# Kernel tuning notes

Hardware: AMD Instinct MI355X
Metric: run time of the kernel (lower is better)

The kernel has to match this reference:

```python
import jax, jax.numpy as jnp
import numpy as np
import math

B, N, DIM, H, D, M = 2, 2048, 512, 8, 64, 128  # batch, seq, model dim, heads, head_dim, num_features


def _sample_orf(head_dim, num_features, seed=0):
    """Orthogonal random features with chi(d) norm scaling (FAVOR+), numpy host-side."""
    rng = np.random.default_rng(seed)
    blocks = []
    while len(blocks) * head_dim < num_features:
        G = rng.standard_normal((head_dim, head_dim)).astype(np.float32)
        Q, _ = np.linalg.qr(G)
        norms = np.linalg.norm(rng.standard_normal((head_dim, head_dim)).astype(np.float32), axis=1)
        blocks.append(np.diag(norms) @ Q.T)
    return np.concatenate(blocks, axis=0)[:num_features]


def setup_inputs() -> dict:
    key = jax.random.key(0)
    ks = jax.random.split(key, 6)
    inner = H * D
    x = jax.random.normal(ks[0], (B, N, DIM), dtype=jnp.float32)
    s = DIM ** -0.5
    Wq = jax.random.normal(ks[1], (inner, DIM), dtype=jnp.float32) * s
    Wk = jax.random.normal(ks[2], (inner, DIM), dtype=jnp.float32) * s
    Wv = jax.random.normal(ks[3], (inner, DIM), dtype=jnp.float32) * s
    Wo = jax.random.normal(ks[4], (DIM, inner), dtype=jnp.float32) * (inner ** -0.5)
    bo = jax.random.normal(ks[5], (DIM,), dtype=jnp.float32) * 0.01
    omega = jnp.asarray(_sample_orf(D, M), dtype=jnp.float32)  # [M, D]
    return {"x": x, "omega": omega, "Wq": Wq, "Wk": Wk, "Wv": Wv, "Wo": Wo, "bo": bo}


def _phi(x, omega, is_query):
    # x: [B,H,N,D], omega: [M,D] -> [B,H,N,M]
    proj = jnp.einsum('bhnd,md->bhnm', x, omega)
    log_phi = proj - 0.5 * jnp.sum(x * x, axis=-1, keepdims=True)
    if is_query:
        log_phi = log_phi - jnp.max(log_phi, axis=-1, keepdims=True)
    else:
        log_phi = log_phi - jnp.max(log_phi)
    return jnp.exp(log_phi) / math.sqrt(M) + 1e-4


def reference(x, omega, Wq, Wk, Wv, Wo, bo):
    # projections: torch Linear is y = x @ W.T
    q = (x @ Wq.T).reshape(B, N, H, D).transpose(0, 2, 1, 3)  # [B,H,N,D]
    k = (x @ Wk.T).reshape(B, N, H, D).transpose(0, 2, 1, 3)
    v = (x @ Wv.T).reshape(B, N, H, D).transpose(0, 2, 1, 3)
    scale = D ** -0.25
    phi_q = _phi(q * scale, omega, True)   # [B,H,N,M]
    phi_k = _phi(k * scale, omega, False)  # [B,H,N,M]

    # Causal linear attention as a recurrent scan over the sequence; math equals
    # cumsum of einsum('bhnm,bhnd->bhnmd') without the O(N*M*D) intermediate.
    def step(carry, inp):
        kv, ksum = carry                      # [B,H,M,D], [B,H,M]
        pqn, pkn, vn = inp                    # [B,H,M], [B,H,M], [B,H,D]
        kv = kv + pkn[..., None] * vn[:, :, None, :]
        ksum = ksum + pkn
        o = jnp.einsum('bhm,bhmd->bhd', pqn, kv)
        z = 1.0 / (jnp.einsum('bhm,bhm->bh', pqn, ksum) + 1e-6)
        return (kv, ksum), o * z[..., None]

    init = (jnp.zeros((B, H, M, D), x.dtype), jnp.zeros((B, H, M), x.dtype))
    xs = (phi_q.transpose(2, 0, 1, 3), phi_k.transpose(2, 0, 1, 3), v.transpose(2, 0, 1, 3))
    _, outs = jax.lax.scan(step, init, xs)    # outs: [N,B,H,D]
    out = outs.transpose(1, 0, 2, 3).reshape(B, N, H * D)
    return out @ Wo.T + bo
```

## Files before the change

kernel.cpp:

```cpp
#include <hip/hip_runtime.h>
#include <math.h>

#define B_ 2
#define N_ 2048
#define DIM_ 512
#define H_ 8
#define D_ 64
#define M_ 128
#define NC_ 32
#define C_ 64

#define INV_SQRT_M 0.08838834764831845f
#define QK_SCALE 0.35355339059327373f

typedef __attribute__((ext_vector_type(8))) short bf16x8;
typedef __attribute__((ext_vector_type(4))) short bf16x4;
typedef __attribute__((ext_vector_type(4))) float f32x4;

#define MFMA16(a, b, c) __builtin_amdgcn_mfma_f32_16x16x32_bf16((a), (b), (c), 0, 0, 0)

__device__ __forceinline__ short f2bf(float f) {
    union { float f; unsigned u; } x; x.f = f;
    unsigned r = (x.u + 0x7FFFu + ((x.u >> 16) & 1u)) >> 16;
    return (short)r;
}
__device__ __forceinline__ float bf2f(short s) {
    union { unsigned u; float f; } x; x.u = ((unsigned)(unsigned short)s) << 16;
    return x.f;
}
__device__ __forceinline__ unsigned encf(float f) {
    unsigned u = __float_as_uint(f);
    return (u & 0x80000000u) ? ~u : (u | 0x80000000u);
}
__device__ __forceinline__ float decf(unsigned e) {
    unsigned u = (e & 0x80000000u) ? (e & 0x7FFFFFFFu) : ~e;
    return __uint_as_float(u);
}

__device__ __forceinline__ void gl16(void* lds, const void* g) {
    __builtin_amdgcn_global_load_lds(
        (const __attribute__((address_space(1))) unsigned int*)g,
        (__attribute__((address_space(3))) unsigned int*)lds,
        16, 0, 0);
}

__device__ __forceinline__ bf16x8 ld_frag(const short* base, int row0, int k0, int ldk) {
    const int lane = threadIdx.x & 63;
    return *(const bf16x8*)(base + (row0 + (lane & 15)) * ldk + k0 + ((lane >> 4) << 3));
}
__device__ __forceinline__ bf16x8 ld_fragT(const short* base, int col0, int k0, int ldk) {
    const int lane = threadIdx.x & 63;
    const short* p = base + (k0 + ((lane >> 4) << 3)) * ldk + col0 + (lane & 15);
    bf16x8 r;
    #pragma unroll
    for (int i = 0; i < 8; ++i) r[i] = p[i * ldk];
    return r;
}

__global__ __launch_bounds__(256) void prep(
    const float* __restrict__ x, const float* __restrict__ Wk, const float* __restrict__ Wv,
    const float* __restrict__ Wo,
    short* __restrict__ xh, short* __restrict__ xl,
    short* __restrict__ Wch, short* __restrict__ Woh, unsigned* __restrict__ gmaxu)
{
    int i4 = blockIdx.x * 256 + threadIdx.x;
    if (i4 == 0) gmaxu[0] = 0u;
    if (i4 < 524288) {
        float4 v = *(const float4*)(x + (size_t)i4 * 4);
        float a[4] = {v.x, v.y, v.z, v.w};
        bf16x4 hi, lo;
        #pragma unroll
        for (int u = 0; u < 4; ++u) {
            short h = f2bf(a[u]); hi[u] = h; lo[u] = f2bf(a[u] - bf2f(h));
        }
        *(bf16x4*)(xh + (size_t)i4 * 4) = hi;
        *(bf16x4*)(xl + (size_t)i4 * 4) = lo;
    } else if (i4 < 720896) {
        int r = i4 - 524288;
        int widx = r >> 16, off4 = r & 65535;
        const float* src; short* dst; float sc;
        if (widx == 0)      { src = Wk; dst = Wch;          sc = QK_SCALE; }
        else if (widx == 1) { src = Wv; dst = Wch + 262144; sc = 1.f; }
        else                { src = Wo; dst = Woh;          sc = 1.f; }
        float4 v = *(const float4*)(src + (size_t)off4 * 4);
        bf16x4 hi;
        hi[0] = f2bf(v.x * sc); hi[1] = f2bf(v.y * sc);
        hi[2] = f2bf(v.z * sc); hi[3] = f2bf(v.w * sc);
        *(bf16x4*)(dst + (size_t)off4 * 4) = hi;
    }
}

__global__ __launch_bounds__(256) void prep_omw(const float* __restrict__ omega,
    const float* __restrict__ Wq, const float* __restrict__ Wk,
    short* __restrict__ Wch, short* __restrict__ Wcl)
{
    __shared__ float Ws[64][65];
    __shared__ float om[128][64];
    const int t = threadIdx.x;
    const int qk = blockIdx.x >> 6, h = (blockIdx.x >> 3) & 7, cb = blockIdx.x & 7;
    const int col0 = cb * 64;
    const float* W = qk ? Wk : Wq;
    for (int i = t; i < 64 * 64; i += 256) {
        int d = i >> 6, c = i & 63;
        Ws[d][c] = W[(size_t)(h * 64 + d) * 512 + col0 + c] * QK_SCALE;
    }
    for (int i = t; i < 128 * 64; i += 256) om[i >> 6][i & 63] = omega[i];
    __syncthreads();
    const int lane = t & 63, w = t >> 6;
    const int c = col0 + lane;
    float Wcol[64];
    #pragma unroll
    for (int d = 0; d < 64; ++d) Wcol[d] = Ws[d][lane];
    for (int mi = 0; mi < 32; ++mi) {
        int m = w * 32 + mi;
        float acc = 0.f;
        #pragma unroll
        for (int d = 0; d < 64; d += 4) {
            float4 o4 = *(const float4*)&om[m][d];
            acc += o4.x * Wcol[d] + o4.y * Wcol[d+1] + o4.z * Wcol[d+2] + o4.w * Wcol[d+3];
        }
        int row = 1024 + qk * 1024 + h * 128 + m;
        short hi = f2bf(acc);
        Wch[(size_t)row * 512 + c] = hi;
        Wcl[(size_t)row * 512 + c] = f2bf(acc - bf2f(hi));
    }
}

__global__ __launch_bounds__(256) void gemm_fused(
    const short* __restrict__ xh, const short* __restrict__ xl,
    const short* __restrict__ Wch, const short* __restrict__ Wcl,
    short* __restrict__ phiq, short* __restrict__ pkloc,
    short* __restrict__ vbf, float* __restrict__ ssqbuf, float* __restrict__ pmaxp)
{
    __shared__ short Ah[128 * 32];
    __shared__ short Al[128 * 32];
    __shared__ short Bh[128 * 32];
    __shared__ short Bl[128 * 32];
    __shared__ float rmx[128][2];
    const int t = threadIdx.x, lane = t & 63, wave = t >> 6;
    const int wr = wave >> 1, wc = wave & 1;
    const int row0 = blockIdx.x * 128;
    const int by = blockIdx.y;
    const int col0 = by * 128;
    const int l_row = lane >> 2, l_col = (lane & 3) << 3;
    const bool three = (by >= 8);
    f32x4 acc[4][4];
    #pragma unroll
    for (int m = 0; m < 4; ++m)
        #pragma unroll
        for (int n = 0; n < 4; ++n) { f32x4 z = {0.f, 0.f, 0.f, 0.f}; acc[m][n] = z; }
    for (int k0 = 0; k0 < 512; k0 += 32) {
        #pragma unroll
        for (int sub = 0; sub < 2; ++sub) {
            int s = wave * 2 + sub;
            int gr = s * 16 + l_row;
            size_t ga = (size_t)(row0 + gr) * 512 + k0 + l_col;
            size_t gb = (size_t)(col0 + gr) * 512 + k0 + l_col;
            gl16(&Ah[s * 512], xh + ga);
            gl16(&Bh[s * 512], Wch + gb);
            if (three) {
                gl16(&Al[s * 512], xl + ga);
                gl16(&Bl[s * 512], Wcl + gb);
            }
        }
        __syncthreads();
        if (three) {
            bf16x8 bh[4], bl[4];
            #pragma unroll
            for (int n = 0; n < 4; ++n) {
                bh[n] = ld_frag(Bh, wc * 64 + n * 16, 0, 32);
                bl[n] = ld_frag(Bl, wc * 64 + n * 16, 0, 32);
            }
            #pragma unroll
            for (int m = 0; m < 4; ++m) {
                bf16x8 ah = ld_frag(Ah, wr * 64 + m * 16, 0, 32);
                bf16x8 al = ld_frag(Al, wr * 64 + m * 16, 0, 32);
                #pragma unroll
                for (int n = 0; n < 4; ++n) {
                    acc[m][n] = MFMA16(al, bh[n], acc[m][n]);
                    acc[m][n] = MFMA16(ah, bl[n], acc[m][n]);
                    acc[m][n] = MFMA16(ah, bh[n], acc[m][n]);
                }
            }
        } else {
            bf16x8 bh[4];
            #pragma unroll
            for (int n = 0; n < 4; ++n) bh[n] = ld_frag(Bh, wc * 64 + n * 16, 0, 32);
            #pragma unroll
            for (int m = 0; m < 4; ++m) {
                bf16x8 ah = ld_frag(Ah, wr * 64 + m * 16, 0, 32);
                #pragma unroll
                for (int n = 0; n < 4; ++n) acc[m][n] = MFMA16(ah, bh[n], acc[m][n]);
            }
        }
        __syncthreads();
    }
    if (by < 4) {
        const int head = by * 2 + wc;
        #pragma unroll
        for (int m = 0; m < 4; ++m)
            #pragma unroll
            for (int i = 0; i < 4; ++i) {
                float s = 0.f;
                #pragma unroll
                for (int n = 0; n < 4; ++n) { float v2 = acc[m][n][i]; s += v2 * v2; }
                s += __shfl_xor(s, 1); s += __shfl_xor(s, 2);
                s += __shfl_xor(s, 4); s += __shfl_xor(s, 8);
                if ((lane & 15) == 0) {
                    int row = row0 + wr * 64 + m * 16 + ((lane >> 4) << 2) + i;
                    int b = row >> 11, nn = row & 2047;
                    ssqbuf[(b * 8 + head) * 2048 + nn] = s;
                }
            }
    } else if (by < 8) {
        #pragma unroll
        for (int m = 0; m < 4; ++m)
            #pragma unroll
            for (int n = 0; n < 4; ++n)
                #pragma unroll
                for (int i = 0; i < 4; ++i) {
                    int row = row0 + wr * 64 + m * 16 + ((lane >> 4) << 2) + i;
                    int gc = col0 + wc * 64 + n * 16 + (lane & 15);
                    int c = gc - 512, h = c >> 6, d = c & 63;
                    int b = row >> 11, nn = row & 2047;
                    vbf[((size_t)(b * 8 + h) * 2048 + nn) * 64 + d] = f2bf(acc[m][n][i]);
                }
    } else {
        const bool isq = (by < 16);
        const int h = isq ? (by - 8) : (by - 16);
        #pragma unroll
        for (int m = 0; m < 4; ++m)
            #pragma unroll
            for (int i = 0; i < 4; ++i) {
                float mx = fmaxf(fmaxf(acc[m][0][i], acc[m][1][i]),
                                 fmaxf(acc[m][2][i], acc[m][3][i]));
                mx = fmaxf(mx, __shfl_xor(mx, 1));
                mx = fmaxf(mx, __shfl_xor(mx, 2));
                mx = fmaxf(mx, __shfl_xor(mx, 4));
                mx = fmaxf(mx, __shfl_xor(mx, 8));
                if ((lane & 15) == 0)
                    rmx[wr * 64 + m * 16 + ((lane >> 4) << 2) + i][wc] = mx;
            }
        __syncthreads();
        short* dst = isq ? phiq : pkloc;
        #pragma unroll
        for (int m = 0; m < 4; ++m)
            #pragma unroll
            for (int i = 0; i < 4; ++i) {
                int lr = wr * 64 + m * 16 + ((lane >> 4) << 2) + i;
                float fm = fmaxf(rmx[lr][0], rmx[lr][1]);
                int row = row0 + lr;
                int b = row >> 11, nn = row & 2047;
                size_t g = (size_t)(b * 8 + h) * 2048 + nn;
                #pragma unroll
                for (int n = 0; n < 4; ++n) {
                    int mc = wc * 64 + n * 16 + (lane & 15);
                    float e = expf(acc[m][n][i] - fm);
                    float val = isq ? (e * INV_SQRT_M + 1e-4f) : e;
                    dst[g * 128 + mc] = f2bf(val);
                }
                if (!isq && wc == 0 && (lane & 15) == 0) pmaxp[g] = fm;
            }
    }
}

__global__ __launch_bounds__(256) void kmax_reduce(const float* __restrict__ pmaxp,
    const float* __restrict__ ssqbuf, unsigned* __restrict__ gmaxu)
{
    float m = -3.402823466e38f;
    for (int g = blockIdx.x * 256 + threadIdx.x; g < 32768; g += 8192)
        m = fmaxf(m, pmaxp[g] - 0.5f * ssqbuf[g]);
    #pragma unroll
    for (int off = 1; off < 64; off <<= 1) m = fmaxf(m, __shfl_xor(m, off));
    __shared__ float w[4];
    if ((threadIdx.x & 63) == 0) w[threadIdx.x >> 6] = m;
    __syncthreads();
    if (threadIdx.x == 0)
        atomicMax(gmaxu, encf(fmaxf(fmaxf(w[0], w[1]), fmaxf(w[2], w[3]))));
}

__global__ __launch_bounds__(256) void chunk_kv_mfma(
    const short* __restrict__ pkloc, const float* __restrict__ ssqbuf,
    const float* __restrict__ pmaxp, const unsigned* __restrict__ gmaxu,
    const short* __restrict__ v_bf, short* __restrict__ Sbf, float* __restrict__ ksum)
{
    __shared__ short pk_l[64][136];
    __shared__ short v_l[64][72];
    __shared__ float srow[64];
    const int t = threadIdx.x, lane = t & 63, wave = t >> 6;
    const int wr = wave >> 1, wc = wave & 1;
    const int bh = blockIdx.x >> 5, j = blockIdx.x & 31;
    const int n0 = j << 6;
    const float g = decf(gmaxu[0]);
    if (t < 64) {
        int gr = bh * 2048 + n0 + t;
        srow[t] = expf(pmaxp[gr] - 0.5f * ssqbuf[gr] - g) * INV_SQRT_M;
    }
    __syncthreads();
    #pragma unroll
    for (int it = 0; it < 4; ++it) {
        int idx = t + it * 256;
        int r = idx >> 4, c8 = (idx & 15) << 3;
        bf16x8 raw = *(const bf16x8*)(pkloc + ((size_t)(bh * 2048 + n0 + r)) * 128 + c8);
        float s = srow[r];
        bf16x8 o;
        #pragma unroll
        for (int u = 0; u < 8; ++u) o[u] = f2bf(bf2f(raw[u]) * s + 1e-4f);
        *(bf16x8*)&pk_l[r][c8] = o;
    }
    #pragma unroll
    for (int it = 0; it < 2; ++it) {
        int idx = t + it * 256;
        int r = idx >> 3, c8 = (idx & 7) << 3;
        *(bf16x8*)&v_l[r][c8] = *(const bf16x8*)(v_bf + ((size_t)(bh * 2048 + n0 + r)) * 64 + c8);
    }
    __syncthreads();
    f32x4 acc[2][4];
    #pragma unroll
    for (int mi = 0; mi < 2; ++mi)
        #pragma unroll
        for (int ni = 0; ni < 4; ++ni) { f32x4 z = {0.f, 0.f, 0.f, 0.f}; acc[mi][ni] = z; }
    #pragma unroll
    for (int ks = 0; ks < 2; ++ks) {
        bf16x8 a0 = ld_fragT(&v_l[0][0], wr * 32, ks * 32, 72);
        bf16x8 a1 = ld_fragT(&v_l[0][0], wr * 32 + 16, ks * 32, 72);
        #pragma unroll
        for (int ni = 0; ni < 4; ++ni) {
            bf16x8 bb = ld_fragT(&pk_l[0][0], wc * 64 + ni * 16, ks * 32, 136);
            acc[0][ni] = MFMA16(a0, bb, acc[0][ni]);
            acc[1][ni] = MFMA16(a1, bb, acc[1][ni]);
        }
    }
    const size_t sbase = ((size_t)blockIdx.x) << 13;
    #pragma unroll
    for (int mi = 0; mi < 2; ++mi)
        #pragma unroll
        for (int ni = 0; ni < 4; ++ni)
            #pragma unroll
            for (int i = 0; i < 4; ++i) {
                int row = wr * 32 + mi * 16 + ((lane >> 4) << 2) + i;
                int col = wc * 64 + ni * 16 + (lane & 15);
                Sbf[sbase + (size_t)row * 128 + col] = f2bf(acc[mi][ni][i]);
            }
    if (t < 128) {
        float s = 0.f;
        #pragma unroll 8
        for (int n = 0; n < 64; ++n) s += bf2f(pk_l[n][t]);
        ksum[((size_t)blockIdx.x) * 128 + t] = s;
    }
}

__global__ __launch_bounds__(256) void prefix_scan(const short* __restrict__ Sbf,
    const float* __restrict__ ksum, short* __restrict__ STbf, float* __restrict__ kpre)
{
    const int bh = blockIdx.x, y = blockIdx.y, t = threadIdx.x;
    if (y < 32) {
        int e = y * 256 + t;
        size_t base = (size_t)bh * NC_ * 8192 + e;
        float vals[NC_];
        #pragma unroll
        for (int j = 0; j < NC_; ++j) vals[j] = bf2f(Sbf[base + (size_t)j * 8192]);
        float run = 0.f;
        #pragma unroll
        for (int j = 0; j < NC_; ++j) {
            STbf[base + (size_t)j * 8192] = f2bf(run);
            run += vals[j];
        }
    } else if (t < 128) {
        size_t base = (size_t)bh * NC_ * 128 + t;
        float vals[NC_];
        #pragma unroll
        for (int j = 0; j < NC_; ++j) vals[j] = ksum[base + (size_t)j * 128];
        float run = 0.f;
        #pragma unroll
        for (int j = 0; j < NC_; ++j) {
            kpre[base + (size_t)j * 128] = run;
            run += vals[j];
        }
    }
}

__global__ __launch_bounds__(256) void chunk_out_mfma(
    const short* __restrict__ phi_q, const short* __restrict__ pkloc,
    const float* __restrict__ ssqbuf, const float* __restrict__ pmaxp,
    const unsigned* __restrict__ gmaxu,
    const short* __restrict__ v_bf, const short* __restrict__ STbf,
    const float* __restrict__ kpre, short* __restrict__ o_hi, short* __restrict__ o_lo)
{
    __shared__ short pq_l[64][136];
    __shared__ short pkst_l[64][136];
    __shared__ short v_l[64][72];
    __shared__ short a_l[64][72];
    __shared__ float rsum[64][8];
    __shared__ float den[64];
    __shared__ float ksp_l[128];
    __shared__ float srow[64];
    const int t = threadIdx.x, lane = t & 63, wave = t >> 6;
    const int wr = wave >> 1, wc = wave & 1;
    const int bh = blockIdx.x >> 5, j = blockIdx.x & 31;
    const int n0 = j << 6;
    const size_t prow = (size_t)bh * N_ + n0;
    const float g = decf(gmaxu[0]);
    if (t < 64) {
        int gr = bh * 2048 + n0 + t;
        srow[t] = expf(pmaxp[gr] - 0.5f * ssqbuf[gr] - g) * INV_SQRT_M;
    }
    if (t < 128) ksp_l[t] = kpre[((size_t)bh * NC_ + j) * 128 + t];
    __syncthreads();
    #pragma unroll
    for (int it = 0; it < 4; ++it) {
        int idx = t + it * 256;
        int r = idx >> 4, c8 = (idx & 15) << 3;
        *(bf16x8*)&pq_l[r][c8] = *(const bf16x8*)(phi_q + (prow + r) * 128 + c8);
        bf16x8 raw = *(const bf16x8*)(pkloc + (prow + r) * 128 + c8);
        float s = srow[r];
        bf16x8 o;
        #pragma unroll
        for (int u = 0; u < 8; ++u) o[u] = f2bf(bf2f(raw[u]) * s + 1e-4f);
        *(bf16x8*)&pkst_l[r][c8] = o;
    }
    #pragma unroll
    for (int it = 0; it < 2; ++it) {
        int idx = t + it * 256;
        int r = idx >> 3, c8 = (idx & 7) << 3;
        *(bf16x8*)&v_l[r][c8] = *(const bf16x8*)(v_bf + (prow + r) * 64 + c8);
    }
    __syncthreads();
    f32x4 qk[2][2];
    #pragma unroll
    for (int mi = 0; mi < 2; ++mi)
        #pragma unroll
        for (int ni = 0; ni < 2; ++ni) { f32x4 z = {0.f, 0.f, 0.f, 0.f}; qk[mi][ni] = z; }
    #pragma unroll
    for (int ks = 0; ks < 4; ++ks) {
        bf16x8 a0 = ld_frag(&pq_l[0][0], wr * 32, ks * 32, 136);
        bf16x8 a1 = ld_frag(&pq_l[0][0], wr * 32 + 16, ks * 32, 136);
        bf16x8 b0 = ld_frag(&pkst_l[0][0], wc * 32, ks * 32, 136);
        bf16x8 b1 = ld_frag(&pkst_l[0][0], wc * 32 + 16, ks * 32, 136);
        qk[0][0] = MFMA16(a0, b0, qk[0][0]);
        qk[0][1] = MFMA16(a0, b1, qk[0][1]);
        qk[1][0] = MFMA16(a1, b0, qk[1][0]);
        qk[1][1] = MFMA16(a1, b1, qk[1][1]);
    }
    #pragma unroll
    for (int mi = 0; mi < 2; ++mi)
        #pragma unroll
        for (int i = 0; i < 4; ++i) {
            int row = wr * 32 + mi * 16 + ((lane >> 4) << 2) + i;
            float part = 0.f;
            #pragma unroll
            for (int ni = 0; ni < 2; ++ni) {
                int col = wc * 32 + ni * 16 + (lane & 15);
                float val = (col <= row) ? qk[mi][ni][i] : 0.f;
                a_l[row][col] = f2bf(val);
                part += val;
            }
            part += __shfl_xor(part, 1);
            part += __shfl_xor(part, 2);
            part += __shfl_xor(part, 4);
            part += __shfl_xor(part, 8);
            if ((lane & 15) == 0) rsum[row][wc] = part;
        }
    {
        int row = t & 63, qq = t >> 6;
        float s = 0.f;
        #pragma unroll
        for (int m = 0; m < 32; ++m) s += bf2f(pq_l[row][qq * 32 + m]) * ksp_l[qq * 32 + m];
        rsum[row][4 + qq] = s;
    }
    __syncthreads();
    #pragma unroll
    for (int it = 0; it < 4; ++it) {
        int idx = t + it * 256;
        int r = idx >> 4, c8 = (idx & 15) << 3;
        *(bf16x8*)&pkst_l[r][c8] =
            *(const bf16x8*)(STbf + (((size_t)bh * NC_ + j) << 13) + r * 128 + c8);
    }
    if (t < 64) {
        float s = rsum[t][0] + rsum[t][1] + rsum[t][4] + rsum[t][5] + rsum[t][6] + rsum[t][7];
        den[t] = 1.0f / (s + 1e-6f);
    }
    __syncthreads();
    f32x4 oa[2][2];
    #pragma unroll
    for (int mi = 0; mi < 2; ++mi)
        #pragma unroll
        for (int ni = 0; ni < 2; ++ni) { f32x4 z = {0.f, 0.f, 0.f, 0.f}; oa[mi][ni] = z; }
    #pragma unroll
    for (int ks = 0; ks < 2; ++ks) {
        bf16x8 a0 = ld_frag(&a_l[0][0], wr * 32, ks * 32, 72);
        bf16x8 a1 = ld_frag(&a_l[0][0], wr * 32 + 16, ks * 32, 72);
        #pragma unroll
        for (int ni = 0; ni < 2; ++ni) {
            bf16x8 bb = ld_fragT(&v_l[0][0], wc * 32 + ni * 16, ks * 32, 72);
            oa[0][ni] = MFMA16(a0, bb, oa[0][ni]);
            oa[1][ni] = MFMA16(a1, bb, oa[1][ni]);
        }
    }
    #pragma unroll
    for (int ks = 0; ks < 4; ++ks) {
        bf16x8 a0 = ld_frag(&pq_l[0][0], wr * 32, ks * 32, 136);
        bf16x8 a1 = ld_frag(&pq_l[0][0], wr * 32 + 16, ks * 32, 136);
        #pragma unroll
        for (int ni = 0; ni < 2; ++ni) {
            bf16x8 bb = ld_frag(&pkst_l[0][0], wc * 32 + ni * 16, ks * 32, 136);
            oa[0][ni] = MFMA16(a0, bb, oa[0][ni]);
            oa[1][ni] = MFMA16(a1, bb, oa[1][ni]);
        }
    }
    const int b_ = bh >> 3, h = bh & 7;
    #pragma unroll
    for (int mi = 0; mi < 2; ++mi)
        #pragma unroll
        for (int ni = 0; ni < 2; ++ni)
            #pragma unroll
            for (int i = 0; i < 4; ++i) {
                int row = wr * 32 + mi * 16 + ((lane >> 4) << 2) + i;
                int col = wc * 32 + ni * 16 + (lane & 15);
                float val = oa[mi][ni][i] * den[row];
                size_t oi = ((size_t)b_ * N_ + n0 + row) * 512 + h * 64 + col;
                short hi = f2bf(val);
                o_hi[oi] = hi;
                o_lo[oi] = f2bf(val - bf2f(hi));
            }
}

__global__ __launch_bounds__(256) void gemm_out(
    const short* __restrict__ ohi, const short* __restrict__ olo,
    const short* __restrict__ Woh, const float* __restrict__ bo, float* __restrict__ out)
{
    __shared__ short Ah[128 * 32];
    __shared__ short Al[128 * 32];
    __shared__ short Bh[64 * 32];
    const int t = threadIdx.x, lane = t & 63, wave = t >> 6;
    const int row0 = blockIdx.x * 128, col0 = blockIdx.y * 64;
    const int l_row = lane >> 2, l_col = (lane & 3) << 3;
    f32x4 acc[2][4];
    #pragma unroll
    for (int m = 0; m < 2; ++m)
        #pragma unroll
        for (int n = 0; n < 4; ++n) { f32x4 z = {0.f, 0.f, 0.f, 0.f}; acc[m][n] = z; }
    for (int k0 = 0; k0 < 512; k0 += 32) {
        #pragma unroll
        for (int sub = 0; sub < 2; ++sub) {
            int s = wave * 2 + sub;
            int gr = s * 16 + l_row;
            size_t ga = (size_t)(row0 + gr) * 512 + k0 + l_col;
            gl16(&Ah[s * 512], ohi + ga);
            gl16(&Al[s * 512], olo + ga);
        }
        {
            int gr = wave * 16 + l_row;
            size_t gb = (size_t)(col0 + gr) * 512 + k0 + l_col;
            gl16(&Bh[wave * 512], Woh + gb);
        }
        __syncthreads();
        bf16x8 bh[4];
        #pragma unroll
        for (int n = 0; n < 4; ++n) bh[n] = ld_frag(Bh, n * 16, 0, 32);
        #pragma unroll
        for (int m = 0; m < 2; ++m) {
            bf16x8 ah = ld_frag(Ah, wave * 32 + m * 16, 0, 32);
            bf16x8 al = ld_frag(Al, wave * 32 + m * 16, 0, 32);
            #pragma unroll
            for (int n = 0; n < 4; ++n) {
                acc[m][n] = MFMA16(al, bh[n], acc[m][n]);
                acc[m][n] = MFMA16(ah, bh[n], acc[m][n]);
            }
        }
        __syncthreads();
    }
    #pragma unroll
    for (int m = 0; m < 2; ++m)
        #pragma unroll
        for (int n = 0; n < 4; ++n)
            #pragma unroll
            for (int i = 0; i < 4; ++i) {
                int gr = row0 + wave * 32 + m * 16 + ((lane >> 4) << 2) + i;
                int gc = col0 + n * 16 + (lane & 15);
                out[(size_t)gr * 512 + gc] = acc[m][n][i] + bo[gc];
            }
}

extern "C" void kernel_launch(void* const* d_in, const int* in_sizes, int n_in,
                              void* d_out, int out_size, void* d_ws, size_t ws_size,
                              hipStream_t stream) {
    const float* x     = (const float*)d_in[0];
    const float* omega = (const float*)d_in[1];
    const float* Wq    = (const float*)d_in[2];
    const float* Wk    = (const float*)d_in[3];
    const float* Wv    = (const float*)d_in[4];
    const float* Wo    = (const float*)d_in[5];
    const float* bo    = (const float*)d_in[6];
    float* out = (float*)d_out;

    char* w = (char*)d_ws;
    short* xh   = (short*)(w);
    short* xl   = (short*)(w + (4ull  << 20));
    short* Wch  = (short*)(w + (8ull  << 20));
    short* Wcl  = (short*)(w + (11ull << 20));
    short* Woh  = (short*)(w + (14ull << 20));
    short* phiq = (short*)(w + (15ull << 20));
    short* pkloc= (short*)(w + (23ull << 20));
    short* vbf  = (short*)(w + (31ull << 20));
    short* Sbf  = (short*)(w + (35ull << 20));
    short* STbf = (short*)(w + (43ull << 20));
    short* ohi  = (short*)(w + (51ull << 20));
    short* olo  = (short*)(w + (55ull << 20));
    float* ssqb = (float*)(w + (59ull << 20));
    float* pmaxp= (float*)(w + (59ull << 20) + (128ull << 10));
    float* ksum = (float*)(w + (59ull << 20) + (256ull << 10));
    float* kpre = (float*)(w + (59ull << 20) + (512ull << 10));
    unsigned* gmaxu = (unsigned*)(w + (59ull << 20) + (768ull << 10));

    prep<<<2816, 256, 0, stream>>>(x, Wk, Wv, Wo, xh, xl, Wch, Woh, gmaxu);
    prep_omw<<<128, 256, 0, stream>>>(omega, Wq, Wk, Wch, Wcl);
    gemm_fused<<<dim3(32, 24), 256, 0, stream>>>(xh, xl, Wch, Wcl, phiq, pkloc,
                                                 vbf, ssqb, pmaxp);
    kmax_reduce<<<32, 256, 0, stream>>>(pmaxp, ssqb, gmaxu);
    chunk_kv_mfma<<<512, 256, 0, stream>>>(pkloc, ssqb, pmaxp, gmaxu, vbf, Sbf, ksum);
    prefix_scan<<<dim3(16, 33), 256, 0, stream>>>(Sbf, ksum, STbf, kpre);
    chunk_out_mfma<<<512, 256, 0, stream>>>(phiq, pkloc, ssqb, pmaxp, gmaxu,
                                            vbf, STbf, kpre, ohi, olo);
    gemm_out<<<dim3(32, 8), 256, 0, stream>>>(ohi, olo, Woh, bo, out);
}
```

Baseline: 173.6 us.

## Merge prep kernels, transpose LDS tiles, vectorize scan, drop output lo-split

Merges the two prep kernels into one launch. Stores pk and v transposed in LDS so MFMA fragments are read as contiguous 16-byte loads instead of strided scalar gathers. Vectorizes the chunk prefix scan to 8 elements per thread, which shrinks its grid. Drops the hi/lo bf16 split of the attention output, halving the loads and MFMAs in the output GEMM at some cost in precision. The scattered transposed LDS writes may cause bank conflicts.

```diff
diff --git a/kernel.cpp b/kernel.cpp
--- a/kernel.cpp
+++ b/kernel.cpp
@@ -48,81 +48,73 @@
     const int lane = threadIdx.x & 63;
     return *(const bf16x8*)(base + (row0 + (lane & 15)) * ldk + k0 + ((lane >> 4) << 3));
 }
-__device__ __forceinline__ bf16x8 ld_fragT(const short* base, int col0, int k0, int ldk) {
-    const int lane = threadIdx.x & 63;
-    const short* p = base + (k0 + ((lane >> 4) << 3)) * ldk + col0 + (lane & 15);
-    bf16x8 r;
-    #pragma unroll
-    for (int i = 0; i < 8; ++i) r[i] = p[i * ldk];
-    return r;
-}
-
-__global__ __launch_bounds__(256) void prep(
-    const float* __restrict__ x, const float* __restrict__ Wk, const float* __restrict__ Wv,
-    const float* __restrict__ Wo,
+
+__global__ __launch_bounds__(256) void prep_all(
+    const float* __restrict__ x, const float* __restrict__ Wq, const float* __restrict__ Wk,
+    const float* __restrict__ Wv, const float* __restrict__ Wo, const float* __restrict__ omega,
     short* __restrict__ xh, short* __restrict__ xl,
-    short* __restrict__ Wch, short* __restrict__ Woh, unsigned* __restrict__ gmaxu)
-{
-    int i4 = blockIdx.x * 256 + threadIdx.x;
-    if (i4 == 0) gmaxu[0] = 0u;
-    if (i4 < 524288) {
-        float4 v = *(const float4*)(x + (size_t)i4 * 4);
-        float a[4] = {v.x, v.y, v.z, v.w};
-        bf16x4 hi, lo;
-        #pragma unroll
-        for (int u = 0; u < 4; ++u) {
-            short h = f2bf(a[u]); hi[u] = h; lo[u] = f2bf(a[u] - bf2f(h));
-        }
-        *(bf16x4*)(xh + (size_t)i4 * 4) = hi;
-        *(bf16x4*)(xl + (size_t)i4 * 4) = lo;
-    } else if (i4 < 720896) {
-        int r = i4 - 524288;
-        int widx = r >> 16, off4 = r & 65535;
-        const float* src; short* dst; float sc;
-        if (widx == 0)      { src = Wk; dst = Wch;          sc = QK_SCALE; }
-        else if (widx == 1) { src = Wv; dst = Wch + 262144; sc = 1.f; }
-        else                { src = Wo; dst = Woh;          sc = 1.f; }
-        float4 v = *(const float4*)(src + (size_t)off4 * 4);
-        bf16x4 hi;
-        hi[0] = f2bf(v.x * sc); hi[1] = f2bf(v.y * sc);
-        hi[2] = f2bf(v.z * sc); hi[3] = f2bf(v.w * sc);
-        *(bf16x4*)(dst + (size_t)off4 * 4) = hi;
-    }
-}
-
-__global__ __launch_bounds__(256) void prep_omw(const float* __restrict__ omega,
-    const float* __restrict__ Wq, const float* __restrict__ Wk,
-    short* __restrict__ Wch, short* __restrict__ Wcl)
+    short* __restrict__ Wch, short* __restrict__ Wcl,
+    short* __restrict__ Woh, unsigned* __restrict__ gmaxu)
 {
     __shared__ float Ws[64][65];
     __shared__ float om[128][64];
     const int t = threadIdx.x;
-    const int qk = blockIdx.x >> 6, h = (blockIdx.x >> 3) & 7, cb = blockIdx.x & 7;
-    const int col0 = cb * 64;
-    const float* W = qk ? Wk : Wq;
-    for (int i = t; i < 64 * 64; i += 256) {
-        int d = i >> 6, c = i & 63;
-        Ws[d][c] = W[(size_t)(h * 64 + d) * 512 + col0 + c] * QK_SCALE;
-    }
-    for (int i = t; i < 128 * 64; i += 256) om[i >> 6][i & 63] = omega[i];
-    __syncthreads();
-    const int lane = t & 63, w = t >> 6;
-    const int c = col0 + lane;
-    float Wcol[64];
-    #pragma unroll
-    for (int d = 0; d < 64; ++d) Wcol[d] = Ws[d][lane];
-    for (int mi = 0; mi < 32; ++mi) {
-        int m = w * 32 + mi;
-        float acc = 0.f;
-        #pragma unroll
-        for (int d = 0; d < 64; d += 4) {
-            float4 o4 = *(const float4*)&om[m][d];
-            acc += o4.x * Wcol[d] + o4.y * Wcol[d+1] + o4.z * Wcol[d+2] + o4.w * Wcol[d+3];
-        }
-        int row = 1024 + qk * 1024 + h * 128 + m;
-        short hi = f2bf(acc);
-        Wch[(size_t)row * 512 + c] = hi;
-        Wcl[(size_t)row * 512 + c] = f2bf(acc - bf2f(hi));
+    const int bid = blockIdx.x;
+    if (bid < 2816) {
+        int i4 = bid * 256 + t;
+        if (i4 == 0) gmaxu[0] = 0u;
+        if (i4 < 524288) {
+            float4 v = *(const float4*)(x + (size_t)i4 * 4);
+            float a[4] = {v.x, v.y, v.z, v.w};
+            bf16x4 hi, lo;
+            #pragma unroll
+            for (int u = 0; u < 4; ++u) {
+                short h = f2bf(a[u]); hi[u] = h; lo[u] = f2bf(a[u] - bf2f(h));
+            }
+            *(bf16x4*)(xh + (size_t)i4 * 4) = hi;
+            *(bf16x4*)(xl + (size_t)i4 * 4) = lo;
+        } else {
+            int r = i4 - 524288;
+            int widx = r >> 16, off4 = r & 65535;
+            const float* src; short* dst; float sc;
+            if (widx == 0)      { src = Wk; dst = Wch;          sc = QK_SCALE; }
+            else if (widx == 1) { src = Wv; dst = Wch + 262144; sc = 1.f; }
+            else                { src = Wo; dst = Woh;          sc = 1.f; }
+            float4 v = *(const float4*)(src + (size_t)off4 * 4);
+            bf16x4 hi;
+            hi[0] = f2bf(v.x * sc); hi[1] = f2bf(v.y * sc);
+            hi[2] = f2bf(v.z * sc); hi[3] = f2bf(v.w * sc);
+            *(bf16x4*)(dst + (size_t)off4 * 4) = hi;
+        }
+    } else {
+        const int bx = bid - 2816;
+        const int qk = bx >> 6, h = (bx >> 3) & 7, cb = bx & 7;
+        const int col0 = cb * 64;
+        const float* W = qk ? Wk : Wq;
+        for (int i = t; i < 64 * 64; i += 256) {
+            int d = i >> 6, c = i & 63;
+            Ws[d][c] = W[(size_t)(h * 64 + d) * 512 + col0 + c] * QK_SCALE;
+        }
+        for (int i = t; i < 128 * 64; i += 256) om[i >> 6][i & 63] = omega[i];
+        __syncthreads();
+        const int lane = t & 63, w = t >> 6;
+        const int c = col0 + lane;
+        float Wcol[64];
+        #pragma unroll
+        for (int d = 0; d < 64; ++d) Wcol[d] = Ws[d][lane];
+        for (int mi = 0; mi < 32; ++mi) {
+            int m = w * 32 + mi;
+            float acc = 0.f;
+            #pragma unroll
+            for (int d = 0; d < 64; d += 4) {
+                float4 o4 = *(const float4*)&om[m][d];
+                acc += o4.x * Wcol[d] + o4.y * Wcol[d+1] + o4.z * Wcol[d+2] + o4.w * Wcol[d+3];
+            }
+            int row = 1024 + qk * 1024 + h * 128 + m;
+            short hi = f2bf(acc);
+            Wch[(size_t)row * 512 + c] = hi;
+            Wcl[(size_t)row * 512 + c] = f2bf(acc - bf2f(hi));
+        }
     }
 }
 
@@ -284,8 +276,8 @@
     const float* __restrict__ pmaxp, const unsigned* __restrict__ gmaxu,
     const short* __restrict__ v_bf, short* __restrict__ Sbf, float* __restrict__ ksum)
 {
-    __shared__ short pk_l[64][136];
-    __shared__ short v_l[64][72];
+    __shared__ short pk_T[128][66];
+    __shared__ short v_T[64][66];
     __shared__ float srow[64];
     const int t = threadIdx.x, lane = t & 63, wave = t >> 6;
     const int wr = wave >> 1, wc = wave & 1;
@@ -303,16 +295,16 @@
         int r = idx >> 4, c8 = (idx & 15) << 3;
         bf16x8 raw = *(const bf16x8*)(pkloc + ((size_t)(bh * 2048 + n0 + r)) * 128 + c8);
         float s = srow[r];
-        bf16x8 o;
-        #pragma unroll
-        for (int u = 0; u < 8; ++u) o[u] = f2bf(bf2f(raw[u]) * s + 1e-4f);
-        *(bf16x8*)&pk_l[r][c8] = o;
+        #pragma unroll
+        for (int u = 0; u < 8; ++u) pk_T[c8 + u][r] = f2bf(bf2f(raw[u]) * s + 1e-4f);
     }
     #pragma unroll
     for (int it = 0; it < 2; ++it) {
         int idx = t + it * 256;
         int r = idx >> 3, c8 = (idx & 7) << 3;
-        *(bf16x8*)&v_l[r][c8] = *(const bf16x8*)(v_bf + ((size_t)(bh * 2048 + n0 + r)) * 64 + c8);
+        bf16x8 raw = *(const bf16x8*)(v_bf + ((size_t)(bh * 2048 + n0 + r)) * 64 + c8);
+        #pragma unroll
+        for (int u = 0; u < 8; ++u) v_T[c8 + u][r] = raw[u];
     }
     __syncthreads();
     f32x4 acc[2][4];
@@ -322,11 +314,11 @@
         for (int ni = 0; ni < 4; ++ni) { f32x4 z = {0.f, 0.f, 0.f, 0.f}; acc[mi][ni] = z; }
     #pragma unroll
     for (int ks = 0; ks < 2; ++ks) {
-        bf16x8 a0 = ld_fragT(&v_l[0][0], wr * 32, ks * 32, 72);
-        bf16x8 a1 = ld_fragT(&v_l[0][0], wr * 32 + 16, ks * 32, 72);
+        bf16x8 a0 = ld_frag(&v_T[0][0], wr * 32, ks * 32, 66);
+        bf16x8 a1 = ld_frag(&v_T[0][0], wr * 32 + 16, ks * 32, 66);
         #pragma unroll
         for (int ni = 0; ni < 4; ++ni) {
-            bf16x8 bb = ld_fragT(&pk_l[0][0], wc * 64 + ni * 16, ks * 32, 136);
+            bf16x8 bb = ld_frag(&pk_T[0][0], wc * 64 + ni * 16, ks * 32, 66);
             acc[0][ni] = MFMA16(a0, bb, acc[0][ni]);
             acc[1][ni] = MFMA16(a1, bb, acc[1][ni]);
         }
@@ -344,8 +336,12 @@
             }
     if (t < 128) {
         float s = 0.f;
-        #pragma unroll 8
-        for (int n = 0; n < 64; ++n) s += bf2f(pk_l[n][t]);
+        #pragma unroll
+        for (int n8 = 0; n8 < 64; n8 += 8) {
+            bf16x8 v = *(const bf16x8*)&pk_T[t][n8];
+            #pragma unroll
+            for (int u = 0; u < 8; ++u) s += bf2f(v[u]);
+        }
         ksum[((size_t)blockIdx.x) * 128 + t] = s;
     }
 }
@@ -354,28 +350,27 @@
     const float* __restrict__ ksum, short* __restrict__ STbf, float* __restrict__ kpre)
 {
     const int bh = blockIdx.x, y = blockIdx.y, t = threadIdx.x;
-    if (y < 32) {
-        int e = y * 256 + t;
-        size_t base = (size_t)bh * NC_ * 8192 + e;
-        float vals[NC_];
-        #pragma unroll
-        for (int j = 0; j < NC_; ++j) vals[j] = bf2f(Sbf[base + (size_t)j * 8192]);
-        float run = 0.f;
+    if (y < 4) {
+        int e8 = (y * 256 + t) * 8;
+        size_t base = (size_t)bh * NC_ * 8192 + e8;
+        float run[8] = {0.f, 0.f, 0.f, 0.f, 0.f, 0.f, 0.f, 0.f};
         #pragma unroll
         for (int j = 0; j < NC_; ++j) {
-            STbf[base + (size_t)j * 8192] = f2bf(run);
-            run += vals[j];
-        }
-    } else if (t < 128) {
-        size_t base = (size_t)bh * NC_ * 128 + t;
-        float vals[NC_];
-        #pragma unroll
-        for (int j = 0; j < NC_; ++j) vals[j] = ksum[base + (size_t)j * 128];
-        float run = 0.f;
+            bf16x8 v = *(const bf16x8*)(Sbf + base + (size_t)j * 8192);
+            bf16x8 o;
+            #pragma unroll
+            for (int u = 0; u < 8; ++u) { o[u] = f2bf(run[u]); run[u] += bf2f(v[u]); }
+            *(bf16x8*)(STbf + base + (size_t)j * 8192) = o;
+        }
+    } else if (t < 32) {
+        size_t base = (size_t)bh * NC_ * 128 + t * 4;
+        float r0 = 0.f, r1 = 0.f, r2 = 0.f, r3 = 0.f;
         #pragma unroll
         for (int j = 0; j < NC_; ++j) {
-            kpre[base + (size_t)j * 128] = run;
-            run += vals[j];
+            float4 v = *(const float4*)(ksum + base + (size_t)j * 128);
+            float4 o; o.x = r0; o.y = r1; o.z = r2; o.w = r3;
+            *(float4*)(kpre + base + (size_t)j * 128) = o;
+            r0 += v.x; r1 += v.y; r2 += v.z; r3 += v.w;
         }
     }
 }
@@ -385,11 +380,11 @@
     const float* __restrict__ ssqbuf, const float* __restrict__ pmaxp,
     const unsigned* __restrict__ gmaxu,
     const short* __restrict__ v_bf, const short* __restrict__ STbf,
-    const float* __restrict__ kpre, short* __restrict__ o_hi, short* __restrict__ o_lo)
+    const float* __restrict__ kpre, short* __restrict__ o_bf)
 {
     __shared__ short pq_l[64][136];
     __shared__ short pkst_l[64][136];
-    __shared__ short v_l[64][72];
+    __shared__ short v_T[64][66];
     __shared__ short a_l[64][72];
     __shared__ float rsum[64][8];
     __shared__ float den[64];
@@ -423,7 +418,9 @@
     for (int it = 0; it < 2; ++it) {
         int idx = t + it * 256;
         int r = idx >> 3, c8 = (idx & 7) << 3;
-        *(bf16x8*)&v_l[r][c8] = *(const bf16x8*)(v_bf + (prow + r) * 64 + c8);
+        bf16x8 raw = *(const bf16x8*)(v_bf + (prow + r) * 64 + c8);
+        #pragma unroll
+        for (int u = 0; u < 8; ++u) v_T[c8 + u][r] = raw[u];
     }
     __syncthreads();
     f32x4 qk[2][2];
@@ -492,7 +489,7 @@
         bf16x8 a1 = ld_frag(&a_l[0][0], wr * 32 + 16, ks * 32, 72);
         #pragma unroll
         for (int ni = 0; ni < 2; ++ni) {
-            bf16x8 bb = ld_fragT(&v_l[0][0], wc * 32 + ni * 16, ks * 32, 72);
+            bf16x8 bb = ld_frag(&v_T[0][0], wc * 32 + ni * 16, ks * 32, 66);
             oa[0][ni] = MFMA16(a0, bb, oa[0][ni]);
             oa[1][ni] = MFMA16(a1, bb, oa[1][ni]);
         }
@@ -519,18 +516,15 @@
                 int col = wc * 32 + ni * 16 + (lane & 15);
                 float val = oa[mi][ni][i] * den[row];
                 size_t oi = ((size_t)b_ * N_ + n0 + row) * 512 + h * 64 + col;
-                short hi = f2bf(val);
-                o_hi[oi] = hi;
-                o_lo[oi] = f2bf(val - bf2f(hi));
+                o_bf[oi] = f2bf(val);
             }
 }
 
 __global__ __launch_bounds__(256) void gemm_out(
-    const short* __restrict__ ohi, const short* __restrict__ olo,
-    const short* __restrict__ Woh, const float* __restrict__ bo, float* __restrict__ out)
+    const short* __restrict__ o_bf, const short* __restrict__ Woh,
+    const float* __restrict__ bo, float* __restrict__ out)
 {
     __shared__ short Ah[128 * 32];
-    __shared__ short Al[128 * 32];
     __shared__ short Bh[64 * 32];
     const int t = threadIdx.x, lane = t & 63, wave = t >> 6;
     const int row0 = blockIdx.x * 128, col0 = blockIdx.y * 64;
@@ -546,8 +540,7 @@
             int s = wave * 2 + sub;
             int gr = s * 16 + l_row;
             size_t ga = (size_t)(row0 + gr) * 512 + k0 + l_col;
-            gl16(&Ah[s * 512], ohi + ga);
-            gl16(&Al[s * 512], olo + ga);
+            gl16(&Ah[s * 512], o_bf + ga);
         }
         {
             int gr = wave * 16 + l_row;
@@ -561,12 +554,9 @@
         #pragma unroll
         for (int m = 0; m < 2; ++m) {
             bf16x8 ah = ld_frag(Ah, wave * 32 + m * 16, 0, 32);
-            bf16x8 al = ld_frag(Al, wave * 32 + m * 16, 0, 32);
-            #pragma unroll
-            for (int n = 0; n < 4; ++n) {
-                acc[m][n] = MFMA16(al, bh[n], acc[m][n]);
+            #pragma unroll
+            for (int n = 0; n < 4; ++n)
                 acc[m][n] = MFMA16(ah, bh[n], acc[m][n]);
-            }
         }
         __syncthreads();
     }
@@ -605,22 +595,21 @@
     short* vbf  = (short*)(w + (31ull << 20));
     short* Sbf  = (short*)(w + (35ull << 20));
     short* STbf = (short*)(w + (43ull << 20));
-    short* ohi  = (short*)(w + (51ull << 20));
-    short* olo  = (short*)(w + (55ull << 20));
+    short* obf  = (short*)(w + (51ull << 20));
     float* ssqb = (float*)(w + (59ull << 20));
     float* pmaxp= (float*)(w + (59ull << 20) + (128ull << 10));
     float* ksum = (float*)(w + (59ull << 20) + (256ull << 10));
     float* kpre = (float*)(w + (59ull << 20) + (512ull << 10));
     unsigned* gmaxu = (unsigned*)(w + (59ull << 20) + (768ull << 10));
 
-    prep<<<2816, 256, 0, stream>>>(x, Wk, Wv, Wo, xh, xl, Wch, Woh, gmaxu);
-    prep_omw<<<128, 256, 0, stream>>>(omega, Wq, Wk, Wch, Wcl);
+    prep_all<<<2944, 256, 0, stream>>>(x, Wq, Wk, Wv, Wo, omega,
+                                       xh, xl, Wch, Wcl, Woh, gmaxu);
     gemm_fused<<<dim3(32, 24), 256, 0, stream>>>(xh, xl, Wch, Wcl, phiq, pkloc,
                                                  vbf, ssqb, pmaxp);
     kmax_reduce<<<32, 256, 0, stream>>>(pmaxp, ssqb, gmaxu);
     chunk_kv_mfma<<<512, 256, 0, stream>>>(pkloc, ssqb, pmaxp, gmaxu, vbf, Sbf, ksum);
-    prefix_scan<<<dim3(16, 33), 256, 0, stream>>>(Sbf, ksum, STbf, kpre);
+    prefix_scan<<<dim3(16, 5), 256, 0, stream>>>(Sbf, ksum, STbf, kpre);
     chunk_out_mfma<<<512, 256, 0, stream>>>(phiq, pkloc, ssqb, pmaxp, gmaxu,
-                                            vbf, STbf, kpre, ohi, olo);
-    gemm_out<<<dim3(32, 8), 256, 0, stream>>>(ohi, olo, Woh, bo, out);
-}
+                                            vbf, STbf, kpre, obf);
+    gemm_out<<<dim3(32, 8), 256, 0, stream>>>(obf, Woh, bo, out);
+}
```

After: 177.5 us. +2.3%, slower.
